# Kernel tuning notes

Hardware: AMD Instinct MI355X
Metric: run time of the kernel (lower is better)

## Reference

```python
import jax, jax.numpy as jnp
import numpy as np

B, T, I, H = 64, 1024, 512, 512


def setup_inputs() -> dict:
    key = jax.random.key(0)
    ks = jax.random.split(key, 9)
    s_i = 1.0 / np.sqrt(I)
    s_h = 1.0 / np.sqrt(H)
    return {
        "x": jax.random.normal(ks[0], (B, T, I), dtype=jnp.float32),
        "h_0": jnp.zeros((B, H), dtype=jnp.float32),
        "W_ir": jax.random.normal(ks[1], (H, I), dtype=jnp.float32) * s_i,
        "W_iz": jax.random.normal(ks[2], (H, I), dtype=jnp.float32) * s_i,
        "W_in": jax.random.normal(ks[3], (H, I), dtype=jnp.float32) * s_i,
        "W_hr": jax.random.normal(ks[4], (H, H), dtype=jnp.float32) * s_h,
        "W_hz": jax.random.normal(ks[5], (H, H), dtype=jnp.float32) * s_h,
        "W_hn": jax.random.normal(ks[6], (H, H), dtype=jnp.float32) * s_h,
        "b_hr": jax.random.normal(ks[7], (H,), dtype=jnp.float32) * s_h,
        "b_hz": jax.random.normal(ks[8], (H,), dtype=jnp.float32) * s_h,
        "b_hn": jax.random.normal(jax.random.fold_in(key, 99), (H,), dtype=jnp.float32) * s_h,
    }


def reference(x, h_0, W_ir, W_iz, W_in, W_hr, W_hz, W_hn, b_hr, b_hz, b_hn):
    # Hoist input-side projections out of the recurrence: three big GEMMs.
    # (B,T,I) @ (I,H) -> (B,T,H), then move time to leading axis for scan.
    xr = jnp.einsum('bti,hi->tbh', x, W_ir)
    xz = jnp.einsum('bti,hi->tbh', x, W_iz)
    xn = jnp.einsum('bti,hi->tbh', x, W_in)

    def step(h, inp):
        xr_t, xz_t, xn_t = inp
        r = jax.nn.sigmoid(xr_t + h @ W_hr.T + b_hr)
        z = jax.nn.sigmoid(xz_t + h @ W_hz.T + b_hz)
        n = jnp.tanh(xn_t + (r * h) @ W_hn.T + b_hn)
        # NOTE: source uses h_t = (1-z)*h + z*n (roles of z swapped vs cuDNN GRU)
        h_new = (1.0 - z) * h + z * n
        return h_new, h_new

    h_n, outs = jax.lax.scan(step, h_0, (xr, xz, xn))  # outs: (T,B,H)
    outputs = jnp.transpose(outs, (1, 0, 2))  # (B,T,H)
    return outputs, h_n
```

## Files before the change

### kernel.cpp

```cpp
#include <hip/hip_runtime.h>
#include <cstddef>
#include <cstdint>


#define NWG 32

typedef __attribute__((ext_vector_type(8))) short bf16x8;
typedef __attribute__((ext_vector_type(4))) float f32x4;

__device__ inline unsigned short f2bf(float f) {
  unsigned int u = __float_as_uint(f);
  unsigned int r = (u + 0x7fffu + ((u >> 16) & 1u)) >> 16;
  return (unsigned short)r;
}
__device__ inline float bf2f(unsigned short s) {
  return __uint_as_float(((unsigned int)s) << 16);
}
__device__ inline bf16x8 as_bf(uint4 v) {
  union { uint4 u; bf16x8 b; } x; x.u = v; return x.b;
}
__device__ inline float sigm(float x) {
  x = fminf(fmaxf(x, -30.f), 30.f);
  return 1.f / (1.f + __expf(-x));
}
__device__ inline float tanhfast(float x) {
  x = fminf(fmaxf(x, -15.f), 15.f);
  float e = __expf(-2.f * x);
  return (1.f - e) / (1.f + e);
}

__device__ inline void pub16(unsigned short* dst, uint4 v) {
  union { uint4 u; unsigned long long q[2]; } x; x.u = v;
  unsigned long long* d = (unsigned long long*)dst;
  __hip_atomic_store(d + 0, x.q[0], __ATOMIC_RELAXED, __HIP_MEMORY_SCOPE_AGENT);
  __hip_atomic_store(d + 1, x.q[1], __ATOMIC_RELAXED, __HIP_MEMORY_SCOPE_AGENT);
}
__device__ inline uint4 rd16(const unsigned short* src) {
  const unsigned long long* s = (const unsigned long long*)src;
  unsigned long long a = __hip_atomic_load(s + 0, __ATOMIC_RELAXED, __HIP_MEMORY_SCOPE_AGENT);
  unsigned long long b = __hip_atomic_load(s + 1, __ATOMIC_RELAXED, __HIP_MEMORY_SCOPE_AGENT);
  union { unsigned long long q[2]; uint4 u; } x; x.q[0] = a; x.q[1] = b;
  return x.u;
}

__global__ void prep_kernel(const float* Wir, const float* Wiz, const float* Win,
                            const float* Whr, const float* Whz, const float* Whn,
                            unsigned short* wfrag, int* bar) {
  const float* Ws[6] = {Wir, Wiz, Win, Whr, Whz, Whn};
  int idx = blockIdx.x * 256 + threadIdx.x;
  if (idx < 6 * 262144) {
    int g = idx >> 18;
    int r = idx & 262143;
    int i = r & 7, lane = (r >> 3) & 63, kt = (r >> 9) & 15, jt = r >> 13;
    int n = lane & 15, q = lane >> 4;
    int j = jt * 16 + n, k = kt * 32 + q * 8 + i;
    wfrag[idx] = f2bf(Ws[g][j * 512 + k]);
  } else {
    int z = idx - 6 * 262144;
    if (z < 4096) bar[z] = 0;
  }
}

__global__ __launch_bounds__(256) void proj_kernel(const float* __restrict__ x,
                                                   const unsigned short* __restrict__ wfrag,
                                                   unsigned short* __restrict__ xslab) {
  __shared__ __align__(16) unsigned short As[64 * 520];
  int bid = blockIdx.x;
  int mLow = bid & 7, j8 = (bid >> 3) & 7, mHigh = bid >> 6;
  int mt = mHigh * 8 + mLow;
  int j0 = j8 * 64;
  int bb = mt >> 4, t0 = (mt & 15) << 6;
  const float* xbase = x + ((size_t)bb * 1024 + t0) * 512;
  for (int c = threadIdx.x; c < 64 * 128; c += 256) {
    int row = c >> 7, f4 = c & 127;
    float4 v = *((const float4*)(xbase + row * 512 + f4 * 4));
    ushort4 o;
    o.x = f2bf(v.x); o.y = f2bf(v.y); o.z = f2bf(v.z); o.w = f2bf(v.w);
    *((ushort4*)(As + row * 520 + f4 * 4)) = o;
  }
  __syncthreads();
  int lane = threadIdx.x & 63, w = threadIdx.x >> 6;
  int nn = lane & 15, qq = lane >> 4;
  for (int gate = 0; gate < 3; ++gate) {
    const unsigned short* wb = wfrag + (size_t)gate * 262144;
    f32x4 acc0 = {0.f,0.f,0.f,0.f}, acc1 = {0.f,0.f,0.f,0.f};
    f32x4 acc2 = {0.f,0.f,0.f,0.f}, acc3 = {0.f,0.f,0.f,0.f};
#pragma unroll
    for (int kt = 0; kt < 16; ++kt) {
      bf16x8 a = *((const bf16x8*)(As + (w * 16 + nn) * 520 + kt * 32 + qq * 8));
      uint4 b0 = *((const uint4*)(wb + (((size_t)(j8 * 4 + 0) * 16 + kt) * 64 + lane) * 8));
      uint4 b1 = *((const uint4*)(wb + (((size_t)(j8 * 4 + 1) * 16 + kt) * 64 + lane) * 8));
      uint4 b2 = *((const uint4*)(wb + (((size_t)(j8 * 4 + 2) * 16 + kt) * 64 + lane) * 8));
      uint4 b3 = *((const uint4*)(wb + (((size_t)(j8 * 4 + 3) * 16 + kt) * 64 + lane) * 8));
      acc0 = __builtin_amdgcn_mfma_f32_16x16x32_bf16(a, as_bf(b0), acc0, 0, 0, 0);
      acc1 = __builtin_amdgcn_mfma_f32_16x16x32_bf16(a, as_bf(b1), acc1, 0, 0, 0);
      acc2 = __builtin_amdgcn_mfma_f32_16x16x32_bf16(a, as_bf(b2), acc2, 0, 0, 0);
      acc3 = __builtin_amdgcn_mfma_f32_16x16x32_bf16(a, as_bf(b3), acc3, 0, 0, 0);
    }
    unsigned short* outs = xslab + (size_t)gate * 33554432;
    f32x4 accs[4] = {acc0, acc1, acc2, acc3};
#pragma unroll
    for (int jt = 0; jt < 4; ++jt) {
#pragma unroll
      for (int r = 0; r < 4; ++r) {
        int t = t0 + w * 16 + qq * 4 + r;
        int j = j0 + jt * 16 + nn;
        outs[(size_t)t * 32768 + bb * 512 + j] = f2bf(accs[jt][r]);
      }
    }
  }
}

__device__ inline void flag_release(int* flags, int wg, int seq) {
  __syncthreads();
  asm volatile("" ::: "memory");
  if (threadIdx.x == 0)
    __hip_atomic_store(flags + wg * 16, seq, __ATOMIC_RELAXED, __HIP_MEMORY_SCOPE_AGENT);
}
__device__ inline void flag_wait(int* flags, int seq) {
  if (threadIdx.x < NWG) {
    const int* f = flags + threadIdx.x * 16;
    while (__hip_atomic_load(f, __ATOMIC_RELAXED, __HIP_MEMORY_SCOPE_AGENT) < seq) {}
  }
  __syncthreads();
  asm volatile("" ::: "memory");
}

__global__ __launch_bounds__(256) void scan_kernel(
    const unsigned short* __restrict__ wfragH, const unsigned short* __restrict__ xslab,
    const float* __restrict__ h0, const float* __restrict__ bhr,
    const float* __restrict__ bhz, const float* __restrict__ bhn,
    float* __restrict__ out, unsigned short* hfrag, unsigned short* rhfrag, int* bar) {
  __shared__ __align__(16) unsigned short whf[3 * 8192];
  __shared__ __align__(16) unsigned short xstage[2][3 * 64 * 16];
  __shared__ float hloc[64 * 17];
  __shared__ __align__(16) unsigned short rhst[64 * 16];
  __shared__ __align__(16) unsigned short hst[64 * 16];
  const int g = blockIdx.x, tid = threadIdx.x;
  const int lane = tid & 63, w = tid >> 6;
  const int nn = lane & 15, qq = lane >> 4;

  const int gate0 = tid >> 7, sub0 = tid & 127, xb0 = sub0 >> 1, xh0 = sub0 & 1;
  const size_t xg0 = (size_t)gate0 * 33554432 + xb0 * 512 + g * 16 + xh0 * 8;
  const int xl0 = (gate0 * 64 + xb0) * 16 + xh0 * 8;
  const int xb1 = tid >> 1, xh1 = tid & 1;
  const size_t xg1 = (size_t)2 * 33554432 + xb1 * 512 + g * 16 + xh1 * 8;
  const int xl1 = (2 * 64 + xb1) * 16 + xh1 * 8;
  uint4 xpf0 = {0,0,0,0}, xpf1 = {0,0,0,0};

  for (int c = tid; c < 3 * 1024; c += 256) {
    int gate = c >> 10, chunk = c & 1023;
    *((uint4*)(whf + gate * 8192 + chunk * 8)) =
        *((const uint4*)(wfragH + (size_t)gate * 262144 + (size_t)g * 8192 + chunk * 8));
  }
  {
    int b = tid >> 2, c = tid & 3;
    float4 v = *((const float4*)(h0 + b * 512 + g * 16 + c * 4));
    hloc[b * 17 + c * 4 + 0] = v.x; hloc[b * 17 + c * 4 + 1] = v.y;
    hloc[b * 17 + c * 4 + 2] = v.z; hloc[b * 17 + c * 4 + 3] = v.w;
  }
  if (tid < 128) {
    int b = tid >> 1, q = tid & 1;
    int k0 = g * 16 + q * 8;
    float4 v0 = *((const float4*)(h0 + b * 512 + k0));
    float4 v1 = *((const float4*)(h0 + b * 512 + k0 + 4));
    union { unsigned short s[8]; uint4 v; } u;
    u.s[0] = f2bf(v0.x); u.s[1] = f2bf(v0.y); u.s[2] = f2bf(v0.z); u.s[3] = f2bf(v0.w);
    u.s[4] = f2bf(v1.x); u.s[5] = f2bf(v1.y); u.s[6] = f2bf(v1.z); u.s[7] = f2bf(v1.w);
    int mt = b >> 4, ktg = g >> 1, qg = ((g & 1) << 1) | q;
    int lg = (b & 15) | (qg << 4);
    pub16(hfrag + ((size_t)(mt * 16 + ktg) * 64 + lg) * 8, u.v);
  }
  xpf0 = *((const uint4*)(xslab + xg0));
  if (tid < 128) xpf1 = *((const uint4*)(xslab + xg1));
  *((uint4*)(&xstage[0][xl0])) = xpf0;
  if (tid < 128) *((uint4*)(&xstage[0][xl1])) = xpf1;

  const float br = bhr[g * 16 + nn], bz = bhz[g * 16 + nn], bn = bhn[g * 16 + nn];
  int sq = 1;
  flag_release(bar, g, sq);
  flag_wait(bar, sq);
  ++sq;

  for (int t = 0; t < 1024; ++t) {
    const unsigned short* xs = xstage[t & 1];
    if (t < 1023) {
      xpf0 = *((const uint4*)(xslab + (size_t)(t + 1) * 32768 + xg0));
      if (tid < 128) xpf1 = *((const uint4*)(xslab + (size_t)(t + 1) * 32768 + xg1));
    }

    f32x4 ar = {0.f,0.f,0.f,0.f}, az = {0.f,0.f,0.f,0.f};
    uint4 af[16];
#pragma unroll
    for (int kt = 0; kt < 16; ++kt)
      af[kt] = rd16(hfrag + ((size_t)(w * 16 + kt) * 64 + lane) * 8);
#pragma unroll
    for (int kt = 0; kt < 16; ++kt) {
      bf16x8 a = as_bf(af[kt]);
      bf16x8 b0 = *((const bf16x8*)(whf + 0 * 8192 + (kt * 64 + lane) * 8));
      bf16x8 b1 = *((const bf16x8*)(whf + 1 * 8192 + (kt * 64 + lane) * 8));
      ar = __builtin_amdgcn_mfma_f32_16x16x32_bf16(a, b0, ar, 0, 0, 0);
      az = __builtin_amdgcn_mfma_f32_16x16x32_bf16(a, b1, az, 0, 0, 0);
    }
    float zv[4];
#pragma unroll
    for (int r = 0; r < 4; ++r) {
      int b = w * 16 + qq * 4 + r;
      float xr = bf2f(xs[(0 * 64 + b) * 16 + nn]);
      float xz = bf2f(xs[(1 * 64 + b) * 16 + nn]);
      float rv = sigm(ar[r] + xr + br);
      zv[r] = sigm(az[r] + xz + bz);
      rhst[b * 16 + nn] = f2bf(rv * hloc[b * 17 + nn]);
    }
    __syncthreads();
    if (tid < 128) {
      int b = tid >> 1, q = tid & 1;
      int mt = b >> 4, ktg = g >> 1, qg = ((g & 1) << 1) | q;
      int lg = (b & 15) | (qg << 4);
      pub16(rhfrag + ((size_t)(mt * 16 + ktg) * 64 + lg) * 8,
            *((const uint4*)(rhst + b * 16 + q * 8)));
    }
    flag_release(bar, g, sq);
    flag_wait(bar, sq);
    ++sq;

    f32x4 an = {0.f,0.f,0.f,0.f};
#pragma unroll
    for (int kt = 0; kt < 16; ++kt)
      af[kt] = rd16(rhfrag + ((size_t)(w * 16 + kt) * 64 + lane) * 8);
#pragma unroll
    for (int kt = 0; kt < 16; ++kt) {
      bf16x8 a = as_bf(af[kt]);
      bf16x8 b2 = *((const bf16x8*)(whf + 2 * 8192 + (kt * 64 + lane) * 8));
      an = __builtin_amdgcn_mfma_f32_16x16x32_bf16(a, b2, an, 0, 0, 0);
    }
    float hv[4];
#pragma unroll
    for (int r = 0; r < 4; ++r) {
      int b = w * 16 + qq * 4 + r;
      float xn = bf2f(xs[(2 * 64 + b) * 16 + nn]);
      float nv = tanhfast(an[r] + xn + bn);
      float ho = hloc[b * 17 + nn];
      float hn = (1.f - zv[r]) * ho + zv[r] * nv;
      hloc[b * 17 + nn] = hn;
      hv[r] = hn;
      hst[b * 16 + nn] = f2bf(hn);
    }
    __syncthreads();
    if (tid < 128) {
      int b = tid >> 1, q = tid & 1;
      int mt = b >> 4, ktg = g >> 1, qg = ((g & 1) << 1) | q;
      int lg = (b & 15) | (qg << 4);
      pub16(hfrag + ((size_t)(mt * 16 + ktg) * 64 + lg) * 8,
            *((const uint4*)(hst + b * 16 + q * 8)));
    }
    flag_release(bar, g, sq);
#pragma unroll
    for (int r = 0; r < 4; ++r) {
      int b = w * 16 + qq * 4 + r;
      out[((size_t)b * 1024 + t) * 512 + g * 16 + nn] = hv[r];
      if (t == 1023) out[(size_t)33554432 + b * 512 + g * 16 + nn] = hv[r];
    }
    if (t < 1023) {
      unsigned short* xw = xstage[(t + 1) & 1];
      *((uint4*)(&xw[xl0])) = xpf0;
      if (tid < 128) *((uint4*)(&xw[xl1])) = xpf1;
    }
    flag_wait(bar, sq);
    ++sq;
  }
}

extern "C" void kernel_launch(void* const* d_in, const int* in_sizes, int n_in,
                              void* d_out, int out_size, void* d_ws, size_t ws_size,
                              hipStream_t stream) {
  (void)in_sizes; (void)n_in; (void)out_size; (void)ws_size;
  const float* x   = (const float*)d_in[0];
  const float* h0  = (const float*)d_in[1];
  const float* Wir = (const float*)d_in[2];
  const float* Wiz = (const float*)d_in[3];
  const float* Win = (const float*)d_in[4];
  const float* Whr = (const float*)d_in[5];
  const float* Whz = (const float*)d_in[6];
  const float* Whn = (const float*)d_in[7];
  const float* bhr = (const float*)d_in[8];
  const float* bhz = (const float*)d_in[9];
  const float* bhn = (const float*)d_in[10];
  float* out = (float*)d_out;
  char* w = (char*)d_ws;
  unsigned short* wfrag  = (unsigned short*)w;
  unsigned short* xslab  = (unsigned short*)(w + 3145728);
  unsigned short* hfrag  = (unsigned short*)(w + 204472320);
  unsigned short* rhfrag = (unsigned short*)(w + 204537856);
  int* bar = (int*)(w + 204603392);

  hipLaunchKernelGGL(prep_kernel, dim3(6160), dim3(256), 0, stream,
                     Wir, Wiz, Win, Whr, Whz, Whn, wfrag, bar);
  hipLaunchKernelGGL(proj_kernel, dim3(8192), dim3(256), 0, stream,
                     x, wfrag, xslab);
  hipLaunchKernelGGL(scan_kernel, dim3(NWG), dim3(256), 0, stream,
                     wfrag + (size_t)3 * 262144, xslab, h0, bhr, bhz, bhn,
                     out, hfrag, rhfrag, bar);
}
```

Before: 6.607 ms.

## Replace workgroup-wide flag barriers with per-wavefront flags and register state

Splits synchronisation by batch tile so that each wavefront publishes its own slice of h and r*h and polls only the 32 flags for its batch tile. This removes the __syncthreads-based release/wait and the cross-wave dependency on every step. Hidden state moves from LDS into registers, and the x projections are loaded per lane straight into registers instead of being double-buffered through LDS. The flag array grows to four times as many slots. Per-lane 2-byte x loads are less coalesced, and the per-wave vmcnt drains before each flag store add latency on the critical path.

After: 7.297 ms. 1.1x slower.

```diff
diff --git a/kernel.cpp b/kernel.cpp
--- a/kernel.cpp
+++ b/kernel.cpp
@@ -41,6 +41,34 @@
   unsigned long long b = __hip_atomic_load(s + 1, __ATOMIC_RELAXED, __HIP_MEMORY_SCOPE_AGENT);
   union { unsigned long long q[2]; uint4 u; } x; x.q[0] = a; x.q[1] = b;
   return x.u;
+}
+
+__device__ inline void lds_fence() {
+  asm volatile("s_waitcnt lgkmcnt(0)" ::: "memory");
+  __builtin_amdgcn_sched_barrier(0);
+}
+__device__ inline void vm_drain() {
+  asm volatile("s_waitcnt vmcnt(0)" ::: "memory");
+  __builtin_amdgcn_sched_barrier(0);
+}
+
+__device__ inline void pollflags(const int* base, int lane, int seq) {
+  const int* f = base + (size_t)(lane & 31) * 16;
+  while (__any(__hip_atomic_load(f, __ATOMIC_RELAXED, __HIP_MEMORY_SCOPE_AGENT) < seq)) {}
+  asm volatile("" ::: "memory");
+  __builtin_amdgcn_sched_barrier(0);
+}
+
+__device__ inline void xload(const unsigned short* __restrict__ xslab, size_t xb,
+                             int t, unsigned short* uxr, unsigned short* uxz,
+                             unsigned short* uxn) {
+  const unsigned short* xp = xslab + (size_t)t * 32768 + xb;
+#pragma unroll
+  for (int r = 0; r < 4; ++r) {
+    uxr[r] = xp[r * 512];
+    uxz[r] = xp[33554432 + (size_t)r * 512];
+    uxn[r] = xp[67108864 + (size_t)r * 512];
+  }
 }
 
 __global__ void prep_kernel(const float* Wir, const float* Wiz, const float* Win,
@@ -111,89 +139,67 @@
   }
 }
 
-__device__ inline void flag_release(int* flags, int wg, int seq) {
-  __syncthreads();
-  asm volatile("" ::: "memory");
-  if (threadIdx.x == 0)
-    __hip_atomic_store(flags + wg * 16, seq, __ATOMIC_RELAXED, __HIP_MEMORY_SCOPE_AGENT);
-}
-__device__ inline void flag_wait(int* flags, int seq) {
-  if (threadIdx.x < NWG) {
-    const int* f = flags + threadIdx.x * 16;
-    while (__hip_atomic_load(f, __ATOMIC_RELAXED, __HIP_MEMORY_SCOPE_AGENT) < seq) {}
-  }
-  __syncthreads();
-  asm volatile("" ::: "memory");
-}
-
 __global__ __launch_bounds__(256) void scan_kernel(
     const unsigned short* __restrict__ wfragH, const unsigned short* __restrict__ xslab,
     const float* __restrict__ h0, const float* __restrict__ bhr,
     const float* __restrict__ bhz, const float* __restrict__ bhn,
     float* __restrict__ out, unsigned short* hfrag, unsigned short* rhfrag, int* bar) {
   __shared__ __align__(16) unsigned short whf[3 * 8192];
-  __shared__ __align__(16) unsigned short xstage[2][3 * 64 * 16];
-  __shared__ float hloc[64 * 17];
-  __shared__ __align__(16) unsigned short rhst[64 * 16];
-  __shared__ __align__(16) unsigned short hst[64 * 16];
+  __shared__ __align__(16) unsigned short stg[4 * 256];
   const int g = blockIdx.x, tid = threadIdx.x;
   const int lane = tid & 63, w = tid >> 6;
   const int nn = lane & 15, qq = lane >> 4;
-
-  const int gate0 = tid >> 7, sub0 = tid & 127, xb0 = sub0 >> 1, xh0 = sub0 & 1;
-  const size_t xg0 = (size_t)gate0 * 33554432 + xb0 * 512 + g * 16 + xh0 * 8;
-  const int xl0 = (gate0 * 64 + xb0) * 16 + xh0 * 8;
-  const int xb1 = tid >> 1, xh1 = tid & 1;
-  const size_t xg1 = (size_t)2 * 33554432 + xb1 * 512 + g * 16 + xh1 * 8;
-  const int xl1 = (2 * 64 + xb1) * 16 + xh1 * 8;
-  uint4 xpf0 = {0,0,0,0}, xpf1 = {0,0,0,0};
 
   for (int c = tid; c < 3 * 1024; c += 256) {
     int gate = c >> 10, chunk = c & 1023;
     *((uint4*)(whf + gate * 8192 + chunk * 8)) =
         *((const uint4*)(wfragH + (size_t)gate * 262144 + (size_t)g * 8192 + chunk * 8));
   }
-  {
-    int b = tid >> 2, c = tid & 3;
-    float4 v = *((const float4*)(h0 + b * 512 + g * 16 + c * 4));
-    hloc[b * 17 + c * 4 + 0] = v.x; hloc[b * 17 + c * 4 + 1] = v.y;
-    hloc[b * 17 + c * 4 + 2] = v.z; hloc[b * 17 + c * 4 + 3] = v.w;
-  }
-  if (tid < 128) {
-    int b = tid >> 1, q = tid & 1;
-    int k0 = g * 16 + q * 8;
+
+  float hreg[4];
+#pragma unroll
+  for (int r = 0; r < 4; ++r)
+    hreg[r] = h0[(w * 16 + qq * 4 + r) * 512 + g * 16 + nn];
+
+  const float br = bhr[g * 16 + nn], bz = bhz[g * 16 + nn], bn = bhn[g * 16 + nn];
+
+  const int prow = lane >> 1, pq = lane & 1;
+  const int ktg = g >> 1, qg = ((g & 1) << 1) | pq;
+  const int plg = prow | (qg << 4);
+  const size_t pdst = ((size_t)(w * 16 + ktg) * 64 + plg) * 8;
+
+  if (lane < 32) {
+    int b = w * 16 + prow, k0 = g * 16 + pq * 8;
     float4 v0 = *((const float4*)(h0 + b * 512 + k0));
     float4 v1 = *((const float4*)(h0 + b * 512 + k0 + 4));
     union { unsigned short s[8]; uint4 v; } u;
     u.s[0] = f2bf(v0.x); u.s[1] = f2bf(v0.y); u.s[2] = f2bf(v0.z); u.s[3] = f2bf(v0.w);
     u.s[4] = f2bf(v1.x); u.s[5] = f2bf(v1.y); u.s[6] = f2bf(v1.z); u.s[7] = f2bf(v1.w);
-    int mt = b >> 4, ktg = g >> 1, qg = ((g & 1) << 1) | q;
-    int lg = (b & 15) | (qg << 4);
-    pub16(hfrag + ((size_t)(mt * 16 + ktg) * 64 + lg) * 8, u.v);
-  }
-  xpf0 = *((const uint4*)(xslab + xg0));
-  if (tid < 128) xpf1 = *((const uint4*)(xslab + xg1));
-  *((uint4*)(&xstage[0][xl0])) = xpf0;
-  if (tid < 128) *((uint4*)(&xstage[0][xl1])) = xpf1;
-
-  const float br = bhr[g * 16 + nn], bz = bhz[g * 16 + nn], bn = bhn[g * 16 + nn];
-  int sq = 1;
-  flag_release(bar, g, sq);
-  flag_wait(bar, sq);
-  ++sq;
+    pub16(hfrag + pdst, u.v);
+  }
+  vm_drain();
+  if (lane == 0)
+    __hip_atomic_store(bar + (w * 32 + g) * 16, 1, __ATOMIC_RELAXED, __HIP_MEMORY_SCOPE_AGENT);
+
+  const size_t xb = (size_t)(w * 16 + qq * 4) * 512 + g * 16 + nn;
+  unsigned short uxr[4], uxz[4], uxn[4];
+  xload(xslab, xb, 0, uxr, uxz, uxn);
+
+  __syncthreads();
+
+  int* const hfl  = bar + w * 512;
+  int* const rhfl = bar + 2048 + w * 512;
+  int* const myh  = bar + (w * 32 + g) * 16;
+  int* const myrh = bar + 2048 + (w * 32 + g) * 16;
+  unsigned short* const stgw = stg + w * 256;
 
   for (int t = 0; t < 1024; ++t) {
-    const unsigned short* xs = xstage[t & 1];
-    if (t < 1023) {
-      xpf0 = *((const uint4*)(xslab + (size_t)(t + 1) * 32768 + xg0));
-      if (tid < 128) xpf1 = *((const uint4*)(xslab + (size_t)(t + 1) * 32768 + xg1));
-    }
-
-    f32x4 ar = {0.f,0.f,0.f,0.f}, az = {0.f,0.f,0.f,0.f};
+    pollflags(hfl, lane, t + 1);
     uint4 af[16];
 #pragma unroll
     for (int kt = 0; kt < 16; ++kt)
       af[kt] = rd16(hfrag + ((size_t)(w * 16 + kt) * 64 + lane) * 8);
+    f32x4 ar = {0.f,0.f,0.f,0.f}, az = {0.f,0.f,0.f,0.f};
 #pragma unroll
     for (int kt = 0; kt < 16; ++kt) {
       bf16x8 a = as_bf(af[kt]);
@@ -205,29 +211,22 @@
     float zv[4];
 #pragma unroll
     for (int r = 0; r < 4; ++r) {
-      int b = w * 16 + qq * 4 + r;
-      float xr = bf2f(xs[(0 * 64 + b) * 16 + nn]);
-      float xz = bf2f(xs[(1 * 64 + b) * 16 + nn]);
-      float rv = sigm(ar[r] + xr + br);
-      zv[r] = sigm(az[r] + xz + bz);
-      rhst[b * 16 + nn] = f2bf(rv * hloc[b * 17 + nn]);
-    }
-    __syncthreads();
-    if (tid < 128) {
-      int b = tid >> 1, q = tid & 1;
-      int mt = b >> 4, ktg = g >> 1, qg = ((g & 1) << 1) | q;
-      int lg = (b & 15) | (qg << 4);
-      pub16(rhfrag + ((size_t)(mt * 16 + ktg) * 64 + lg) * 8,
-            *((const uint4*)(rhst + b * 16 + q * 8)));
-    }
-    flag_release(bar, g, sq);
-    flag_wait(bar, sq);
-    ++sq;
-
-    f32x4 an = {0.f,0.f,0.f,0.f};
+      float rv = sigm(ar[r] + bf2f(uxr[r]) + br);
+      zv[r] = sigm(az[r] + bf2f(uxz[r]) + bz);
+      stgw[(qq * 4 + r) * 16 + nn] = f2bf(rv * hreg[r]);
+    }
+    lds_fence();
+    if (lane < 32)
+      pub16(rhfrag + pdst, *((const uint4*)(stgw + prow * 16 + pq * 8)));
+    vm_drain();
+    if (lane == 0)
+      __hip_atomic_store(myrh, t + 1, __ATOMIC_RELAXED, __HIP_MEMORY_SCOPE_AGENT);
+
+    pollflags(rhfl, lane, t + 1);
 #pragma unroll
     for (int kt = 0; kt < 16; ++kt)
       af[kt] = rd16(rhfrag + ((size_t)(w * 16 + kt) * 64 + lane) * 8);
+    f32x4 an = {0.f,0.f,0.f,0.f};
 #pragma unroll
     for (int kt = 0; kt < 16; ++kt) {
       bf16x8 a = as_bf(af[kt]);
@@ -237,37 +236,26 @@
     float hv[4];
 #pragma unroll
     for (int r = 0; r < 4; ++r) {
-      int b = w * 16 + qq * 4 + r;
-      float xn = bf2f(xs[(2 * 64 + b) * 16 + nn]);
-      float nv = tanhfast(an[r] + xn + bn);
-      float ho = hloc[b * 17 + nn];
-      float hn = (1.f - zv[r]) * ho + zv[r] * nv;
-      hloc[b * 17 + nn] = hn;
+      float nv = tanhfast(an[r] + bf2f(uxn[r]) + bn);
+      float hn = (1.f - zv[r]) * hreg[r] + zv[r] * nv;
+      hreg[r] = hn;
       hv[r] = hn;
-      hst[b * 16 + nn] = f2bf(hn);
-    }
-    __syncthreads();
-    if (tid < 128) {
-      int b = tid >> 1, q = tid & 1;
-      int mt = b >> 4, ktg = g >> 1, qg = ((g & 1) << 1) | q;
-      int lg = (b & 15) | (qg << 4);
-      pub16(hfrag + ((size_t)(mt * 16 + ktg) * 64 + lg) * 8,
-            *((const uint4*)(hst + b * 16 + q * 8)));
-    }
-    flag_release(bar, g, sq);
+      stgw[(qq * 4 + r) * 16 + nn] = f2bf(hn);
+    }
+    lds_fence();
+    if (lane < 32)
+      pub16(hfrag + pdst, *((const uint4*)(stgw + prow * 16 + pq * 8)));
+    vm_drain();
+    if (lane == 0)
+      __hip_atomic_store(myh, t + 2, __ATOMIC_RELAXED, __HIP_MEMORY_SCOPE_AGENT);
+
 #pragma unroll
     for (int r = 0; r < 4; ++r) {
       int b = w * 16 + qq * 4 + r;
       out[((size_t)b * 1024 + t) * 512 + g * 16 + nn] = hv[r];
       if (t == 1023) out[(size_t)33554432 + b * 512 + g * 16 + nn] = hv[r];
     }
-    if (t < 1023) {
-      unsigned short* xw = xstage[(t + 1) & 1];
-      *((uint4*)(&xw[xl0])) = xpf0;
-      if (tid < 128) *((uint4*)(&xw[xl1])) = xpf1;
-    }
-    flag_wait(bar, sq);
-    ++sq;
+    if (t < 1023) xload(xslab, xb, t + 1, uxr, uxz, uxn);
   }
 }
 
```
